# Optimization experiments

Hardware: AMD Instinct MI355X
Metric: run time of the kernel (lower is better)

## Reference

```python
import jax, jax.numpy as jnp
import numpy as np

DIM = 512
HEADS = 8
DIM_HEAD = 64
DIM_INNER = HEADS * DIM_HEAD
NULL_KV = 2
CD_ITERS = 50
CD_K = 8.0
CD_EPS = 0.1
LN_EPS = 1e-5


def setup_inputs() -> dict:
    key = jax.random.key(0)
    k0, k1, k2, k3 = jax.random.split(key, 4)
    b, n = 1, 1024
    x = jax.random.normal(k0, (b, n, DIM), dtype=jnp.float32)
    w_qkv = jax.random.normal(k1, (DIM, 3 * DIM_INNER), dtype=jnp.float32) * (DIM ** -0.5)
    w_out = jax.random.normal(k2, (DIM_INNER, DIM), dtype=jnp.float32) * (DIM_INNER ** -0.5)
    null_kv = jax.random.normal(k3, (2, HEADS, NULL_KV, DIM_HEAD), dtype=jnp.float32)
    ln_g = jnp.ones((DIM,), dtype=jnp.float32)
    ln_b = jnp.zeros((DIM,), dtype=jnp.float32)
    return {"x": x, "w_qkv": w_qkv, "w_out": w_out, "null_kv": null_kv,
            "ln_g": ln_g, "ln_b": ln_b}


def _coor_descent(s, mask, k, n_iters, eps):
    # s: (b, h, i, j); mask True = attend. eps_decay==1 upstream => eps fixed.
    mask_value = -jnp.finfo(s.dtype).max
    logk = jnp.log(jnp.asarray(k, dtype=s.dtype))
    s = jnp.where(mask, s, mask_value)

    def step(carry, _):
        a, b = carry
        sb = jnp.where(mask, (s + b) / eps, mask_value)
        a = eps * (logk - jax.nn.logsumexp(sb, axis=-1, keepdims=True))
        b = -jax.nn.relu(-s - a)
        return (a, b), None

    a0 = jnp.zeros(s.shape[:-1] + (1,), dtype=s.dtype)
    b0 = -s
    (a, b), _ = jax.lax.scan(jax.checkpoint(step), (a0, b0), None, length=n_iters)
    scores = jnp.exp((s + a + b) / eps)
    return jnp.where(mask, scores, 0.0)


def reference(x, w_qkv, w_out, null_kv, ln_g, ln_b):
    b, n, _ = x.shape
    # LayerNorm (biased variance, torch default eps)
    mu = jnp.mean(x, axis=-1, keepdims=True)
    var = jnp.var(x, axis=-1, keepdims=True)
    xn = (x - mu) / jnp.sqrt(var + LN_EPS) * ln_g + ln_b

    qkv = xn @ w_qkv                                  # (b, n, 3*dim_inner)
    q, k, v = jnp.split(qkv, 3, axis=-1)
    to_heads = lambda t: t.reshape(b, n, HEADS, DIM_HEAD).transpose(0, 2, 1, 3)
    q, k, v = to_heads(q), to_heads(k), to_heads(v)   # (b, h, n, d)

    nk = jnp.broadcast_to(null_kv[0], (b, HEADS, NULL_KV, DIM_HEAD))
    nv = jnp.broadcast_to(null_kv[1], (b, HEADS, NULL_KV, DIM_HEAD))
    k = jnp.concatenate([nk, k], axis=-2)             # (b, h, n+nkv, d)
    v = jnp.concatenate([nv, v], axis=-2)

    q = q * (DIM_HEAD ** -0.5)
    sim = jnp.einsum('bhid,bhjd->bhij', q, k)         # (b, h, i, j)
    i, j = sim.shape[-2:]
    causal = jnp.triu(jnp.ones((i, j), dtype=bool), j - i + 1)
    mask = ~causal                                    # True = attend (null kv always visible)

    attn = _coor_descent(sim, mask, CD_K, CD_ITERS, CD_EPS)
    out = jnp.einsum('bhij,bhjd->bhid', attn, v)
    out = out.transpose(0, 2, 1, 3).reshape(b, n, DIM_INNER)
    return out @ w_out
```

## Files before the change

### kernel.cpp

```cpp
#include <hip/hip_runtime.h>
#include <math.h>

#define NHEAD 8
#define SROW 1088
#define PSTR 1088
#define VSTR 1056
#define LOGK 2.0794415416798357f

typedef __bf16 bf16x8 __attribute__((ext_vector_type(8)));
typedef __bf16 bf16x4 __attribute__((ext_vector_type(4)));
typedef float  f32x4  __attribute__((ext_vector_type(4)));

__device__ __forceinline__ void split2(float v, __bf16& hi, __bf16& lo) {
    hi = (__bf16)v; lo = (__bf16)(v - (float)hi);
}

__device__ __forceinline__ float dpp_sum64(float x) {
    int v;
    v = __builtin_amdgcn_update_dpp(0, __float_as_int(x), 0x111, 0xf, 0xf, true); x += __int_as_float(v);
    v = __builtin_amdgcn_update_dpp(0, __float_as_int(x), 0x112, 0xf, 0xf, true); x += __int_as_float(v);
    v = __builtin_amdgcn_update_dpp(0, __float_as_int(x), 0x114, 0xf, 0xf, true); x += __int_as_float(v);
    v = __builtin_amdgcn_update_dpp(0, __float_as_int(x), 0x118, 0xf, 0xf, true); x += __int_as_float(v);
    v = __builtin_amdgcn_update_dpp(0, __float_as_int(x), 0x142, 0xa, 0xf, true); x += __int_as_float(v);
    v = __builtin_amdgcn_update_dpp(0, __float_as_int(x), 0x143, 0xc, 0xf, true); x += __int_as_float(v);
    return __int_as_float(__builtin_amdgcn_readlane(__float_as_int(x), 63));
}
__device__ __forceinline__ float dpp_max64(float x) {
    int v;
    v = __builtin_amdgcn_update_dpp(__float_as_int(x), __float_as_int(x), 0x111, 0xf, 0xf, false); x = fmaxf(x, __int_as_float(v));
    v = __builtin_amdgcn_update_dpp(__float_as_int(x), __float_as_int(x), 0x112, 0xf, 0xf, false); x = fmaxf(x, __int_as_float(v));
    v = __builtin_amdgcn_update_dpp(__float_as_int(x), __float_as_int(x), 0x114, 0xf, 0xf, false); x = fmaxf(x, __int_as_float(v));
    v = __builtin_amdgcn_update_dpp(__float_as_int(x), __float_as_int(x), 0x118, 0xf, 0xf, false); x = fmaxf(x, __int_as_float(v));
    v = __builtin_amdgcn_update_dpp(__float_as_int(x), __float_as_int(x), 0x142, 0xa, 0xf, false); x = fmaxf(x, __int_as_float(v));
    v = __builtin_amdgcn_update_dpp(__float_as_int(x), __float_as_int(x), 0x143, 0xc, 0xf, false); x = fmaxf(x, __int_as_float(v));
    return __int_as_float(__builtin_amdgcn_readlane(__float_as_int(x), 63));
}

__global__ __launch_bounds__(256) void prep_kernel(const float* __restrict__ x,
                                                   const float* __restrict__ g,
                                                   const float* __restrict__ bb,
                                                   const float* __restrict__ w_qkv,
                                                   const float* __restrict__ w_out,
                                                   const float* __restrict__ nkv,
                                                   __bf16* __restrict__ xnh,
                                                   __bf16* __restrict__ xnl,
                                                   __bf16* __restrict__ wqh,
                                                   __bf16* __restrict__ wql,
                                                   __bf16* __restrict__ wo,
                                                   __bf16* __restrict__ kh,
                                                   __bf16* __restrict__ kl,
                                                   __bf16* __restrict__ vT) {
    __shared__ float T[64][65];
    __shared__ float sm[2][4];
    int b = blockIdx.x, tid = threadIdx.x;

    if (b < 512) {
        int half = tid >> 7, t = tid & 127;
        int row = (b << 1) + half;
        float4 v = ((const float4*)(x + (size_t)row * 512))[t];
        float s  = v.x + v.y + v.z + v.w;
        float ss = fmaf(v.x, v.x, fmaf(v.y, v.y, fmaf(v.z, v.z, v.w * v.w)));
#pragma unroll
        for (int off = 32; off; off >>= 1) {
            s  += __shfl_down(s, off);
            ss += __shfl_down(ss, off);
        }
        int wih = (tid >> 6) & 1;
        if ((tid & 63) == 0) { sm[half][wih * 2] = s; sm[half][wih * 2 + 1] = ss; }
        __syncthreads();
        s = sm[half][0] + sm[half][2]; ss = sm[half][1] + sm[half][3];
        float mu   = s * (1.f / 512);
        float var  = ss * (1.f / 512) - mu * mu;
        float rstd = 1.f / sqrtf(var + 1e-5f);
        float4 gv = ((const float4*)g)[t];
        float4 bv = ((const float4*)bb)[t];
        float o[4];
        o[0] = (v.x - mu) * rstd * gv.x + bv.x;
        o[1] = (v.y - mu) * rstd * gv.y + bv.y;
        o[2] = (v.z - mu) * rstd * gv.z + bv.z;
        o[3] = (v.w - mu) * rstd * gv.w + bv.w;
        bf16x4 h4, l4;
#pragma unroll
        for (int e = 0; e < 4; ++e) { __bf16 hi, lo; split2(o[e], hi, lo); h4[e] = hi; l4[e] = lo; }
        *(bf16x4*)(xnh + (size_t)row * 512 + t * 4) = h4;
        *(bf16x4*)(xnl + (size_t)row * 512 + t * 4) = l4;
    } else if (b < 704) {
        int b2 = b - 512;
        int k0 = (b2 & 7) * 64, n0 = (b2 >> 3) * 64;
        int r = tid >> 2, c0 = (tid & 3) << 4;
#pragma unroll
        for (int u = 0; u < 4; ++u) {
            float4 w = *(const float4*)(w_qkv + (size_t)(k0 + r) * 1536 + n0 + c0 + 4 * u);
            T[r][c0 + 4 * u + 0] = w.x; T[r][c0 + 4 * u + 1] = w.y;
            T[r][c0 + 4 * u + 2] = w.z; T[r][c0 + 4 * u + 3] = w.w;
        }
        __syncthreads();
        int nr = tid >> 2, kc0 = (tid & 3) << 4;
#pragma unroll
        for (int u = 0; u < 4; ++u) {
            bf16x4 h4, l4;
#pragma unroll
            for (int e = 0; e < 4; ++e) {
                __bf16 hi, lo; split2(T[kc0 + 4 * u + e][nr], hi, lo);
                h4[e] = hi; l4[e] = lo;
            }
            *(bf16x4*)(wqh + (size_t)(n0 + nr) * 512 + k0 + kc0 + 4 * u) = h4;
            *(bf16x4*)(wql + (size_t)(n0 + nr) * 512 + k0 + kc0 + 4 * u) = l4;
        }
    } else if (b < 768) {
        int b2 = b - 704;
        int k0 = (b2 & 7) * 64, n0 = (b2 >> 3) * 64;
        int r = tid >> 2, c0 = (tid & 3) << 4;
#pragma unroll
        for (int u = 0; u < 4; ++u) {
            float4 w = *(const float4*)(w_out + (size_t)(k0 + r) * 512 + n0 + c0 + 4 * u);
            T[r][c0 + 4 * u + 0] = w.x; T[r][c0 + 4 * u + 1] = w.y;
            T[r][c0 + 4 * u + 2] = w.z; T[r][c0 + 4 * u + 3] = w.w;
        }
        __syncthreads();
        int nr = tid >> 2, kc0 = (tid & 3) << 4;
#pragma unroll
        for (int u = 0; u < 4; ++u) {
            bf16x4 h4;
#pragma unroll
            for (int e = 0; e < 4; ++e) h4[e] = (__bf16)T[kc0 + 4 * u + e][nr];
            *(bf16x4*)(wo + (size_t)(n0 + nr) * 512 + k0 + kc0 + 4 * u) = h4;
        }
    } else {
        int t2 = (b - 768) * 256 + tid;
        int d = t2 & 63, p = (t2 >> 6) & 1, h = t2 >> 7;
        float kvf = nkv[((0 * NHEAD + h) * 2 + p) * 64 + d];
        __bf16 hi, lo; split2(kvf, hi, lo);
        kh[((size_t)h * SROW + p) * 64 + d] = hi;
        kl[((size_t)h * SROW + p) * 64 + d] = lo;
        float vf = nkv[((NHEAD + h) * 2 + p) * 64 + d];
        vT[((size_t)(h * 64) + d) * VSTR + p] = (__bf16)vf;
        int base = t2 * 15;
#pragma unroll
        for (int e = 0; e < 15; ++e) {
            int z = base + e;
            int jj = 1026 + (z % 30);
            int hd = z / 30;
            vT[(size_t)hd * VSTR + jj] = (__bf16)0.f;
        }
    }
}

__global__ __launch_bounds__(256, 4) void qkv_mfma(const __bf16* __restrict__ xh,
                                                   const __bf16* __restrict__ xl,
                                                   const __bf16* __restrict__ bh,
                                                   const __bf16* __restrict__ bl,
                                                   __bf16* __restrict__ qh,
                                                   __bf16* __restrict__ ql,
                                                   __bf16* __restrict__ kh,
                                                   __bf16* __restrict__ kl,
                                                   __bf16* __restrict__ vT) {
    int tid = threadIdx.x, l = tid & 63, w = tid >> 6;
    int m0 = blockIdx.x * 32, n0 = blockIdx.y * 64;
    int ms = (w & 1) << 4, nh2 = (w >> 1) << 5;
    int arow = m0 + ms + (l & 15);
    f32x4 acc[2] = {};
#pragma unroll 2
    for (int ks = 0; ks < 16; ++ks) {
        int koff = ((l >> 4) << 3) + (ks << 5);
        bf16x8 ah = *(const bf16x8*)(xh + (size_t)arow * 512 + koff);
        bf16x8 al = *(const bf16x8*)(xl + (size_t)arow * 512 + koff);
#pragma unroll
        for (int ct = 0; ct < 2; ++ct) {
            int ncol = n0 + nh2 + (ct << 4) + (l & 15);
            bf16x8 bhv = *(const bf16x8*)(bh + (size_t)ncol * 512 + koff);
            bf16x8 blv = *(const bf16x8*)(bl + (size_t)ncol * 512 + koff);
            acc[ct] = __builtin_amdgcn_mfma_f32_16x16x32_bf16(ah, bhv, acc[ct], 0, 0, 0);
            acc[ct] = __builtin_amdgcn_mfma_f32_16x16x32_bf16(al, bhv, acc[ct], 0, 0, 0);
            acc[ct] = __builtin_amdgcn_mfma_f32_16x16x32_bf16(ah, blv, acc[ct], 0, 0, 0);
        }
    }
#pragma unroll
    for (int ct = 0; ct < 2; ++ct) {
        int c = n0 + nh2 + (ct << 4) + (l & 15);
#pragma unroll
        for (int r = 0; r < 4; ++r) {
            int m = m0 + ms + ((l >> 4) << 2) + r;
            float val = acc[ct][r];
            if (c < 512) {
                int h = c >> 6, d = c & 63;
                __bf16 hi, lo; split2(val * 1.25f, hi, lo);
                qh[(((size_t)(h << 10)) + m) * 64 + d] = hi;
                ql[(((size_t)(h << 10)) + m) * 64 + d] = lo;
            } else if (c < 1024) {
                int c2 = c - 512, h = c2 >> 6, d = c2 & 63;
                __bf16 hi, lo; split2(val, hi, lo);
                kh[((size_t)h * SROW + 2 + m) * 64 + d] = hi;
                kl[((size_t)h * SROW + 2 + m) * 64 + d] = lo;
            } else {
                int c2 = c - 1024, h = c2 >> 6, d = c2 & 63;
                vT[((size_t)(h * 64) + d) * VSTR + 2 + m] = (__bf16)val;
            }
        }
    }
}

__global__ __launch_bounds__(512, 4) void qkcd_kernel(const __bf16* __restrict__ qh,
                                                      const __bf16* __restrict__ ql,
                                                      const __bf16* __restrict__ kh,
                                                      const __bf16* __restrict__ kl,
                                                      __bf16* __restrict__ pbuf) {
    __shared__ float s_lds[1040 * 17];
    int tid = threadIdx.x, l = tid & 63, w = tid >> 6;
    int ip0 = blockIdx.x << 3, h = blockIdx.y;
    int ext = 1026 - ip0;
    int T = (ext + 15) >> 4;

    int c16 = l & 15;
    int kgrp = (l >> 4) << 3;
    int row16 = (c16 < 8) ? (1016 - ip0 + c16) : (ip0 + c16 - 8);
    const __bf16* qrb = qh + ((size_t)(h << 10) + row16) * 64 + kgrp;
    const __bf16* qrl = ql + ((size_t)(h << 10) + row16) * 64 + kgrp;
    bf16x8 qB0 = *(const bf16x8*)(qrb);
    bf16x8 qB1 = *(const bf16x8*)(qrb + 32);
    bf16x8 qL0 = *(const bf16x8*)(qrl);
    bf16x8 qL1 = *(const bf16x8*)(qrl + 32);

    const __bf16* khb = kh + ((size_t)h * SROW) * 64;
    const __bf16* klb = kl + ((size_t)h * SROW) * 64;
    for (int jt = w; jt < T; jt += 8) {
        int jg = (jt << 4) + c16;
        const __bf16* ka = khb + (size_t)jg * 64 + kgrp;
        const __bf16* kb = klb + (size_t)jg * 64 + kgrp;
        f32x4 acc = {};
        bf16x8 ah0 = *(const bf16x8*)(ka);
        bf16x8 al0 = *(const bf16x8*)(kb);
        bf16x8 ah1 = *(const bf16x8*)(ka + 32);
        bf16x8 al1 = *(const bf16x8*)(kb + 32);
        acc = __builtin_amdgcn_mfma_f32_16x16x32_bf16(ah0, qB0, acc, 0, 0, 0);
        acc = __builtin_amdgcn_mfma_f32_16x16x32_bf16(al0, qB0, acc, 0, 0, 0);
        acc = __builtin_amdgcn_mfma_f32_16x16x32_bf16(ah0, qL0, acc, 0, 0, 0);
        acc = __builtin_amdgcn_mfma_f32_16x16x32_bf16(ah1, qB1, acc, 0, 0, 0);
        acc = __builtin_amdgcn_mfma_f32_16x16x32_bf16(al1, qB1, acc, 0, 0, 0);
        acc = __builtin_amdgcn_mfma_f32_16x16x32_bf16(ah1, qL1, acc, 0, 0, 0);
        int jb0 = (jt << 4) + ((l >> 4) << 2);
#pragma unroll
        for (int r = 0; r < 4; ++r)
            s_lds[(jb0 + r) * 17 + c16] = acc[r];
    }
    __syncthreads();

    int ip = ip0 + w;
    int iA = 1023 - ip, iB = ip;
    int nvA = iA + 3, nvB = iB + 3;
    int colA = 7 - w, colB = 8 + w;
    int jb = l << 2;

    float4 EA[5], EB[3];
    float mA = -INFINITY, mB = -INFINITY;
#pragma unroll
    for (int t = 0; t < 5; ++t) {
        float* sp = (float*)&EA[t];
#pragma unroll
        for (int c = 0; c < 4; ++c) {
            int j = jb + c + (t << 8);
            float v = (j < nvA) ? s_lds[j * 17 + colA] : -INFINITY;
            sp[c] = v; mA = fmaxf(mA, v);
        }
    }
#pragma unroll
    for (int t = 0; t < 3; ++t) {
        float* sp = (float*)&EB[t];
#pragma unroll
        for (int c = 0; c < 4; ++c) {
            int j = jb + c + (t << 8);
            float v = (j < nvB) ? s_lds[j * 17 + colB] : -INFINITY;
            sp[c] = v; mB = fmaxf(mB, v);
        }
    }
    mA = dpp_max64(mA); mB = dpp_max64(mB);

#pragma unroll
    for (int t = 0; t < 5; ++t) {
        float* sp = (float*)&EA[t];
#pragma unroll
        for (int c = 0; c < 4; ++c) sp[c] = __expf(sp[c] - mA);
    }
#pragma unroll
    for (int t = 0; t < 3; ++t) {
        float* sp = (float*)&EB[t];
#pragma unroll
        for (int c = 0; c < 4; ++c) sp[c] = __expf(sp[c] - mB);
    }

    float gA = LOGK - __logf((float)nvA) + mA;
    float gB = LOGK - __logf((float)nvB) + mB;
    bool dA = false, dB = false;
#pragma unroll 1
    for (int it = 1; it < 50; ++it) {
        if (!dA) {
            float eg = __expf(fminf(gA, 80.f));
            float a0 = 0.f, a1 = 0.f, a2 = 0.f, a3 = 0.f;
#pragma unroll
            for (int t = 0; t < 5; ++t) {
                float* ep = (float*)&EA[t];
                a0 += ep[0] * fminf(1.f, ep[0] * eg);
                a1 += ep[1] * fminf(1.f, ep[1] * eg);
                a2 += ep[2] * fminf(1.f, ep[2] * eg);
                a3 += ep[3] * fminf(1.f, ep[3] * eg);
            }
            float sum = dpp_sum64((a0 + a1) + (a2 + a3));
            float g2 = LOGK - __logf(sum);
            dA = (__float_as_int(g2) == __float_as_int(gA));
            gA = g2;
        }
        if (!dB) {
            float eg = __expf(fminf(gB, 80.f));
            float b0 = 0.f, b1 = 0.f, b2 = 0.f, b3 = 0.f;
#pragma unroll
            for (int t = 0; t < 3; ++t) {
                float* ep = (float*)&EB[t];
                b0 += ep[0] * fminf(1.f, ep[0] * eg);
                b1 += ep[1] * fminf(1.f, ep[1] * eg);
                b2 += ep[2] * fminf(1.f, ep[2] * eg);
                b3 += ep[3] * fminf(1.f, ep[3] * eg);
            }
            float sum = dpp_sum64((b0 + b1) + (b2 + b3));
            float g2 = LOGK - __logf(sum);
            dB = (__float_as_int(g2) == __float_as_int(gB));
            gB = g2;
        }
        if (dA && dB) break;
    }

    float egA = __expf(fminf(gA, 80.f));
    float egB = __expf(fminf(gB, 80.f));
    __bf16* pA = pbuf + ((size_t)(h << 10) + iA) * PSTR;
    __bf16* pB = pbuf + ((size_t)(h << 10) + iB) * PSTR;
#pragma unroll
    for (int t = 0; t < 5; ++t) {
        if (jb + (t << 8) < PSTR) {
            bf16x4 pv;
            float* ep = (float*)&EA[t];
#pragma unroll
            for (int c = 0; c < 4; ++c) {
                float wv = ep[c] * egA;
                pv[c] = (__bf16)(wv * fminf(1.f, wv));
            }
            *(bf16x4*)(pA + jb + (t << 8)) = pv;
        }
    }
#pragma unroll
    for (int t = 0; t < 3; ++t) {
        bf16x4 pv;
        float* ep = (float*)&EB[t];
#pragma unroll
        for (int c = 0; c < 4; ++c) {
            float wv = ep[c] * egB;
            pv[c] = (__bf16)(wv * fminf(1.f, wv));
        }
        *(bf16x4*)(pB + jb + (t << 8)) = pv;
    }
    bf16x4 z4 = {};
#pragma unroll
    for (int t = 3; t < 5; ++t) {
        if (jb + (t << 8) < PSTR) *(bf16x4*)(pB + jb + (t << 8)) = z4;
    }
}

__global__ __launch_bounds__(256, 4) void pv_mfma(const __bf16* __restrict__ pbuf,
                                                  const __bf16* __restrict__ vT,
                                                  __bf16* __restrict__ ao) {
    int i0 = blockIdx.x << 4, h = blockIdx.y;
    int tid = threadIdx.x, l = tid & 63, w = tid >> 6;
    int arow = i0 + (l & 15);
    int dcol = (w << 4) + (l & 15);
    const __bf16* pr = pbuf + ((size_t)(h << 10) + arow) * PSTR;
    const __bf16* vr = vT + ((size_t)(h << 6) + dcol) * VSTR;
    f32x4 acc0 = {}, acc1 = {};
    int kb = (l >> 4) << 3;
#pragma unroll 4
    for (int ks = 0; ks < 32; ks += 2) {
        bf16x8 a0 = *(const bf16x8*)(pr + kb + (ks << 5));
        bf16x8 b0 = *(const bf16x8*)(vr + kb + (ks << 5));
        bf16x8 a1 = *(const bf16x8*)(pr + kb + ((ks + 1) << 5));
        bf16x8 b1 = *(const bf16x8*)(vr + kb + ((ks + 1) << 5));
        acc0 = __builtin_amdgcn_mfma_f32_16x16x32_bf16(a0, b0, acc0, 0, 0, 0);
        acc1 = __builtin_amdgcn_mfma_f32_16x16x32_bf16(a1, b1, acc1, 0, 0, 0);
    }
    {
        bf16x8 a0 = *(const bf16x8*)(pr + kb + (32 << 5));
        bf16x8 b0 = *(const bf16x8*)(vr + kb + (32 << 5));
        acc0 = __builtin_amdgcn_mfma_f32_16x16x32_bf16(a0, b0, acc0, 0, 0, 0);
    }
#pragma unroll
    for (int r = 0; r < 4; ++r) {
        int i = i0 + ((l >> 4) << 2) + r;
        ao[(size_t)i * 512 + (h << 6) + dcol] = (__bf16)(acc0[r] + acc1[r]);
    }
}

__global__ __launch_bounds__(256, 4) void out_mfma(const __bf16* __restrict__ ao,
                                                   const __bf16* __restrict__ wo,
                                                   float* __restrict__ out) {
    int m0 = blockIdx.x << 4, bn = blockIdx.y;
    int tid = threadIdx.x, l = tid & 63, w = tid >> 6;
    int arow = m0 + (l & 15);
    int ncol = (bn << 6) + (w << 4) + (l & 15);
    const __bf16* ar = ao + (size_t)arow * 512;
    const __bf16* br = wo + (size_t)ncol * 512;
    f32x4 acc0 = {}, acc1 = {};
    int kb = (l >> 4) << 3;
#pragma unroll 4
    for (int ks = 0; ks < 16; ks += 2) {
        bf16x8 a0 = *(const bf16x8*)(ar + kb + (ks << 5));
        bf16x8 b0 = *(const bf16x8*)(br + kb + (ks << 5));
        bf16x8 a1 = *(const bf16x8*)(ar + kb + ((ks + 1) << 5));
        bf16x8 b1 = *(const bf16x8*)(br + kb + ((ks + 1) << 5));
        acc0 = __builtin_amdgcn_mfma_f32_16x16x32_bf16(a0, b0, acc0, 0, 0, 0);
        acc1 = __builtin_amdgcn_mfma_f32_16x16x32_bf16(a1, b1, acc1, 0, 0, 0);
    }
#pragma unroll
    for (int r = 0; r < 4; ++r) {
        int m = m0 + ((l >> 4) << 2) + r;
        out[(size_t)m * 512 + ncol] = acc0[r] + acc1[r];
    }
}

extern "C" void kernel_launch(void* const* d_in, const int* in_sizes, int n_in,
                              void* d_out, int out_size, void* d_ws, size_t ws_size,
                              hipStream_t stream) {
    const float* x      = (const float*)d_in[0];
    const float* w_qkv  = (const float*)d_in[1];
    const float* w_out  = (const float*)d_in[2];
    const float* nullkv = (const float*)d_in[3];
    const float* ln_g   = (const float*)d_in[4];
    const float* ln_b   = (const float*)d_in[5];
    float* ws = (float*)d_ws;
    float* out = (float*)d_out;

    float* base = ws;
    __bf16* xnh = (__bf16*)(base);              base += 262144;
    __bf16* xnl = (__bf16*)(base);              base += 262144;
    __bf16* wqh = (__bf16*)(base);              base += 393216;
    __bf16* wql = (__bf16*)(base);              base += 393216;
    __bf16* qh  = (__bf16*)(base);              base += 262144;
    __bf16* ql  = (__bf16*)(base);              base += 262144;
    __bf16* kh  = (__bf16*)(base);              base += 278528;
    __bf16* kl  = (__bf16*)(base);              base += 278528;
    __bf16* vT  = (__bf16*)(base);              base += 270336;
    __bf16* wo  = (__bf16*)(base);              base += 131072;
    __bf16* ao  = (__bf16*)(base);              base += 262144;
    __bf16* pbuf = (__bf16*)(base);

    hipLaunchKernelGGL(prep_kernel, dim3(772),    dim3(256), 0, stream,
                       x, ln_g, ln_b, w_qkv, w_out, nullkv,
                       xnh, xnl, wqh, wql, wo, kh, kl, vT);
    hipLaunchKernelGGL(qkv_mfma,   dim3(32, 24),  dim3(256), 0, stream, xnh, xnl, wqh, wql, qh, ql, kh, kl, vT);
    hipLaunchKernelGGL(qkcd_kernel, dim3(64, 8),  dim3(512), 0, stream, qh, ql, kh, kl, pbuf);
    hipLaunchKernelGGL(pv_mfma,    dim3(64, 8),   dim3(256), 0, stream, pbuf, vT, ao);
    hipLaunchKernelGGL(out_mfma,   dim3(64, 8),   dim3(256), 0, stream, ao, wo, out);
}
```

Measured before the change: 172.7 us.

## Fuse P·V into coordinate-descent kernel via LDS-resident attention rows

Removes the separate pv_mfma kernel and the global pbuf round-trip: the sparse attention weights for each block's 16 rows are written to LDS (reusing the score buffer) and multiplied by V inside the same kernel, with K split across two wave halves and reduced through LDS. It also skips loading, exponentiating and accumulating register tiles that lie entirely past a row's causal extent. The cost is extra block-wide barriers and heavier per-block work in a kernel already constrained by LDS and registers. V is still read from global memory by every block.

New measurement: 157.9 us. 8.5% less time.

```diff
diff --git a/kernel.cpp b/kernel.cpp
--- a/kernel.cpp
+++ b/kernel.cpp
@@ -3,8 +3,8 @@
 
 #define NHEAD 8
 #define SROW 1088
-#define PSTR 1088
 #define VSTR 1056
+#define PLDS 1064
 #define LOGK 2.0794415416798357f
 
 typedef __bf16 bf16x8 __attribute__((ext_vector_type(8)));
@@ -200,12 +200,16 @@
     }
 }
 
-__global__ __launch_bounds__(512, 4) void qkcd_kernel(const __bf16* __restrict__ qh,
-                                                      const __bf16* __restrict__ ql,
-                                                      const __bf16* __restrict__ kh,
-                                                      const __bf16* __restrict__ kl,
-                                                      __bf16* __restrict__ pbuf) {
+__global__ __launch_bounds__(512, 4) void qkcdpv_kernel(const __bf16* __restrict__ qh,
+                                                        const __bf16* __restrict__ ql,
+                                                        const __bf16* __restrict__ kh,
+                                                        const __bf16* __restrict__ kl,
+                                                        const __bf16* __restrict__ vT,
+                                                        __bf16* __restrict__ ao) {
     __shared__ float s_lds[1040 * 17];
+    __bf16* p_lds  = (__bf16*)s_lds;
+    float*  redbuf = s_lds + 9000;
+
     int tid = threadIdx.x, l = tid & 63, w = tid >> 6;
     int ip0 = blockIdx.x << 3, h = blockIdx.y;
     int ext = 1026 - ip0;
@@ -213,9 +217,9 @@
 
     int c16 = l & 15;
     int kgrp = (l >> 4) << 3;
-    int row16 = (c16 < 8) ? (1016 - ip0 + c16) : (ip0 + c16 - 8);
-    const __bf16* qrb = qh + ((size_t)(h << 10) + row16) * 64 + kgrp;
-    const __bf16* qrl = ql + ((size_t)(h << 10) + row16) * 64 + kgrp;
+    int row16q = (c16 < 8) ? (1016 - ip0 + c16) : (ip0 + c16 - 8);
+    const __bf16* qrb = qh + ((size_t)(h << 10) + row16q) * 64 + kgrp;
+    const __bf16* qrl = ql + ((size_t)(h << 10) + row16q) * 64 + kgrp;
     bf16x8 qB0 = *(const bf16x8*)(qrb);
     bf16x8 qB1 = *(const bf16x8*)(qrb + 32);
     bf16x8 qL0 = *(const bf16x8*)(qrl);
@@ -248,6 +252,7 @@
     int ip = ip0 + w;
     int iA = 1023 - ip, iB = ip;
     int nvA = iA + 3, nvB = iB + 3;
+    int tA = (nvA + 255) >> 8, tB = (nvB + 255) >> 8;
     int colA = 7 - w, colB = 8 + w;
     int jb = l << 2;
 
@@ -256,36 +261,45 @@
 #pragma unroll
     for (int t = 0; t < 5; ++t) {
         float* sp = (float*)&EA[t];
-#pragma unroll
-        for (int c = 0; c < 4; ++c) {
-            int j = jb + c + (t << 8);
-            float v = (j < nvA) ? s_lds[j * 17 + colA] : -INFINITY;
-            sp[c] = v; mA = fmaxf(mA, v);
-        }
+        if (t < tA) {
+#pragma unroll
+            for (int c = 0; c < 4; ++c) {
+                int j = jb + c + (t << 8);
+                float v = (j < nvA) ? s_lds[j * 17 + colA] : -INFINITY;
+                sp[c] = v; mA = fmaxf(mA, v);
+            }
+        } else { sp[0] = sp[1] = sp[2] = sp[3] = 0.f; }
     }
 #pragma unroll
     for (int t = 0; t < 3; ++t) {
         float* sp = (float*)&EB[t];
-#pragma unroll
-        for (int c = 0; c < 4; ++c) {
-            int j = jb + c + (t << 8);
-            float v = (j < nvB) ? s_lds[j * 17 + colB] : -INFINITY;
-            sp[c] = v; mB = fmaxf(mB, v);
-        }
+        if (t < tB) {
+#pragma unroll
+            for (int c = 0; c < 4; ++c) {
+                int j = jb + c + (t << 8);
+                float v = (j < nvB) ? s_lds[j * 17 + colB] : -INFINITY;
+                sp[c] = v; mB = fmaxf(mB, v);
+            }
+        } else { sp[0] = sp[1] = sp[2] = sp[3] = 0.f; }
     }
     mA = dpp_max64(mA); mB = dpp_max64(mB);
+    __syncthreads();
 
 #pragma unroll
     for (int t = 0; t < 5; ++t) {
         float* sp = (float*)&EA[t];
-#pragma unroll
-        for (int c = 0; c < 4; ++c) sp[c] = __expf(sp[c] - mA);
+        if (t < tA) {
+#pragma unroll
+            for (int c = 0; c < 4; ++c) sp[c] = __expf(sp[c] - mA);
+        }
     }
 #pragma unroll
     for (int t = 0; t < 3; ++t) {
         float* sp = (float*)&EB[t];
-#pragma unroll
-        for (int c = 0; c < 4; ++c) sp[c] = __expf(sp[c] - mB);
+        if (t < tB) {
+#pragma unroll
+            for (int c = 0; c < 4; ++c) sp[c] = __expf(sp[c] - mB);
+        }
     }
 
     float gA = LOGK - __logf((float)nvA) + mA;
@@ -298,11 +312,13 @@
             float a0 = 0.f, a1 = 0.f, a2 = 0.f, a3 = 0.f;
 #pragma unroll
             for (int t = 0; t < 5; ++t) {
-                float* ep = (float*)&EA[t];
-                a0 += ep[0] * fminf(1.f, ep[0] * eg);
-                a1 += ep[1] * fminf(1.f, ep[1] * eg);
-                a2 += ep[2] * fminf(1.f, ep[2] * eg);
-                a3 += ep[3] * fminf(1.f, ep[3] * eg);
+                if (t < tA) {
+                    float* ep = (float*)&EA[t];
+                    a0 += ep[0] * fminf(1.f, ep[0] * eg);
+                    a1 += ep[1] * fminf(1.f, ep[1] * eg);
+                    a2 += ep[2] * fminf(1.f, ep[2] * eg);
+                    a3 += ep[3] * fminf(1.f, ep[3] * eg);
+                }
             }
             float sum = dpp_sum64((a0 + a1) + (a2 + a3));
             float g2 = LOGK - __logf(sum);
@@ -314,11 +330,13 @@
             float b0 = 0.f, b1 = 0.f, b2 = 0.f, b3 = 0.f;
 #pragma unroll
             for (int t = 0; t < 3; ++t) {
-                float* ep = (float*)&EB[t];
-                b0 += ep[0] * fminf(1.f, ep[0] * eg);
-                b1 += ep[1] * fminf(1.f, ep[1] * eg);
-                b2 += ep[2] * fminf(1.f, ep[2] * eg);
-                b3 += ep[3] * fminf(1.f, ep[3] * eg);
+                if (t < tB) {
+                    float* ep = (float*)&EB[t];
+                    b0 += ep[0] * fminf(1.f, ep[0] * eg);
+                    b1 += ep[1] * fminf(1.f, ep[1] * eg);
+                    b2 += ep[2] * fminf(1.f, ep[2] * eg);
+                    b3 += ep[3] * fminf(1.f, ep[3] * eg);
+                }
             }
             float sum = dpp_sum64((b0 + b1) + (b2 + b3));
             float g2 = LOGK - __logf(sum);
@@ -328,70 +346,77 @@
         if (dA && dB) break;
     }
 
-    float egA = __expf(fminf(gA, 80.f));
-    float egB = __expf(fminf(gB, 80.f));
-    __bf16* pA = pbuf + ((size_t)(h << 10) + iA) * PSTR;
-    __bf16* pB = pbuf + ((size_t)(h << 10) + iB) * PSTR;
-#pragma unroll
-    for (int t = 0; t < 5; ++t) {
-        if (jb + (t << 8) < PSTR) {
-            bf16x4 pv;
-            float* ep = (float*)&EA[t];
-#pragma unroll
-            for (int c = 0; c < 4; ++c) {
-                float wv = ep[c] * egA;
-                pv[c] = (__bf16)(wv * fminf(1.f, wv));
-            }
-            *(bf16x4*)(pA + jb + (t << 8)) = pv;
-        }
-    }
-#pragma unroll
-    for (int t = 0; t < 3; ++t) {
-        bf16x4 pv;
-        float* ep = (float*)&EB[t];
-#pragma unroll
-        for (int c = 0; c < 4; ++c) {
-            float wv = ep[c] * egB;
-            pv[c] = (__bf16)(wv * fminf(1.f, wv));
-        }
-        *(bf16x4*)(pB + jb + (t << 8)) = pv;
-    }
-    bf16x4 z4 = {};
-#pragma unroll
-    for (int t = 3; t < 5; ++t) {
-        if (jb + (t << 8) < PSTR) *(bf16x4*)(pB + jb + (t << 8)) = z4;
-    }
-}
-
-__global__ __launch_bounds__(256, 4) void pv_mfma(const __bf16* __restrict__ pbuf,
-                                                  const __bf16* __restrict__ vT,
-                                                  __bf16* __restrict__ ao) {
-    int i0 = blockIdx.x << 4, h = blockIdx.y;
-    int tid = threadIdx.x, l = tid & 63, w = tid >> 6;
-    int arow = i0 + (l & 15);
-    int dcol = (w << 4) + (l & 15);
-    const __bf16* pr = pbuf + ((size_t)(h << 10) + arow) * PSTR;
-    const __bf16* vr = vT + ((size_t)(h << 6) + dcol) * VSTR;
-    f32x4 acc0 = {}, acc1 = {};
-    int kb = (l >> 4) << 3;
-#pragma unroll 4
-    for (int ks = 0; ks < 32; ks += 2) {
-        bf16x8 a0 = *(const bf16x8*)(pr + kb + (ks << 5));
-        bf16x8 b0 = *(const bf16x8*)(vr + kb + (ks << 5));
-        bf16x8 a1 = *(const bf16x8*)(pr + kb + ((ks + 1) << 5));
-        bf16x8 b1 = *(const bf16x8*)(vr + kb + ((ks + 1) << 5));
-        acc0 = __builtin_amdgcn_mfma_f32_16x16x32_bf16(a0, b0, acc0, 0, 0, 0);
-        acc1 = __builtin_amdgcn_mfma_f32_16x16x32_bf16(a1, b1, acc1, 0, 0, 0);
-    }
     {
-        bf16x8 a0 = *(const bf16x8*)(pr + kb + (32 << 5));
-        bf16x8 b0 = *(const bf16x8*)(vr + kb + (32 << 5));
-        acc0 = __builtin_amdgcn_mfma_f32_16x16x32_bf16(a0, b0, acc0, 0, 0, 0);
-    }
-#pragma unroll
-    for (int r = 0; r < 4; ++r) {
-        int i = i0 + ((l >> 4) << 2) + r;
-        ao[(size_t)i * 512 + (h << 6) + dcol] = (__bf16)(acc0[r] + acc1[r]);
+        float egA = __expf(fminf(gA, 80.f));
+        float egB = __expf(fminf(gB, 80.f));
+        __bf16* prA = p_lds + (size_t)colA * PLDS;
+        __bf16* prB = p_lds + (size_t)colB * PLDS;
+#pragma unroll
+        for (int t = 0; t < 5; ++t) {
+            int j0 = jb + (t << 8);
+            if (j0 < 1056) {
+                bf16x4 pv;
+                float* ep = (float*)&EA[t];
+#pragma unroll
+                for (int c = 0; c < 4; ++c) {
+                    float wv = ep[c] * egA;
+                    pv[c] = (__bf16)(wv * fminf(1.f, wv));
+                }
+                *(bf16x4*)(prA + j0) = pv;
+            }
+        }
+#pragma unroll
+        for (int t = 0; t < 3; ++t) {
+            int j0 = jb + (t << 8);
+            if (j0 < 1056) {
+                bf16x4 pv;
+                float* ep = (float*)&EB[t];
+#pragma unroll
+                for (int c = 0; c < 4; ++c) {
+                    float wv = ep[c] * egB;
+                    pv[c] = (__bf16)(wv * fminf(1.f, wv));
+                }
+                *(bf16x4*)(prB + j0) = pv;
+            }
+        }
+        bf16x4 z4 = {};
+#pragma unroll
+        for (int t = 3; t < 5; ++t) {
+            int j0 = jb + (t << 8);
+            if (j0 < 1056) *(bf16x4*)(prB + j0) = z4;
+        }
+    }
+    __syncthreads();
+
+    {
+        int dblk = (w & 3) << 4;
+        int dcol = dblk + c16;
+        int khalf = w >> 2;
+        const __bf16* vr = vT + ((size_t)(h << 6) + dcol) * VSTR;
+        const __bf16* pr = p_lds + (size_t)c16 * PLDS;
+        f32x4 acc = {};
+        int ks0 = khalf ? 16 : 0;
+        int ks1 = khalf ? 33 : 16;
+        for (int ks = ks0; ks < ks1; ++ks) {
+            bf16x8 a = *(const bf16x8*)(pr + kgrp + (ks << 5));
+            bf16x8 b = *(const bf16x8*)(vr + kgrp + (ks << 5));
+            acc = __builtin_amdgcn_mfma_f32_16x16x32_bf16(a, b, acc, 0, 0, 0);
+        }
+        if (w >= 4) {
+#pragma unroll
+            for (int r = 0; r < 4; ++r)
+                redbuf[(size_t)(w & 3) * 272 + ((l >> 4) * 4 + r) * 17 + c16] = acc[r];
+        }
+        __syncthreads();
+        if (w < 4) {
+#pragma unroll
+            for (int r = 0; r < 4; ++r) {
+                int row16 = (l >> 4) * 4 + r;
+                float v = acc[r] + redbuf[(size_t)w * 272 + row16 * 17 + c16];
+                int gi = (row16 < 8) ? (1016 - ip0 + row16) : (ip0 + row16 - 8);
+                ao[(size_t)gi * 512 + (h << 6) + dcol] = (__bf16)v;
+            }
+        }
     }
 }
 
@@ -446,13 +471,11 @@
     __bf16* vT  = (__bf16*)(base);              base += 270336;
     __bf16* wo  = (__bf16*)(base);              base += 131072;
     __bf16* ao  = (__bf16*)(base);              base += 262144;
-    __bf16* pbuf = (__bf16*)(base);
 
     hipLaunchKernelGGL(prep_kernel, dim3(772),    dim3(256), 0, stream,
                        x, ln_g, ln_b, w_qkv, w_out, nullkv,
                        xnh, xnl, wqh, wql, wo, kh, kl, vT);
-    hipLaunchKernelGGL(qkv_mfma,   dim3(32, 24),  dim3(256), 0, stream, xnh, xnl, wqh, wql, qh, ql, kh, kl, vT);
-    hipLaunchKernelGGL(qkcd_kernel, dim3(64, 8),  dim3(512), 0, stream, qh, ql, kh, kl, pbuf);
-    hipLaunchKernelGGL(pv_mfma,    dim3(64, 8),   dim3(256), 0, stream, pbuf, vT, ao);
-    hipLaunchKernelGGL(out_mfma,   dim3(64, 8),   dim3(256), 0, stream, ao, wo, out);
-}
+    hipLaunchKernelGGL(qkv_mfma,    dim3(32, 24), dim3(256), 0, stream, xnh, xnl, wqh, wql, qh, ql, kh, kl, vT);
+    hipLaunchKernelGGL(qkcdpv_kernel, dim3(64, 8), dim3(512), 0, stream, qh, ql, kh, kl, vT, ao);
+    hipLaunchKernelGGL(out_mfma,    dim3(64, 8),  dim3(256), 0, stream, ao, wo, out);
+}
```
